# Kernel tuning notes

Measured on AMD Instinct MI355X. Metric: run time of the kernel, lower is better.

Reference implementation:

```python
import jax, jax.numpy as jnp
import numpy as np

C_CURV = 0.01   # manifold curvature c
EPS = 1e-7
KH = KW = 3
PAD = 1
STRIDE = 1


def log0(y):
    # Poincare-ball log map at origin: artanh(sqrt(c)||y||) * y / (sqrt(c)||y||)
    sqc = jnp.sqrt(jnp.asarray(C_CURV, y.dtype))
    n = jnp.maximum(jnp.linalg.norm(y, axis=-1, keepdims=True), EPS)
    return jnp.arctanh(jnp.clip(sqc * n, 0.0, 1.0 - 1e-6)) * y / (sqc * n)


def exp0(v):
    # Poincare-ball exp map at origin: tanh(sqrt(c)||v||) * v / (sqrt(c)||v||)
    sqc = jnp.sqrt(jnp.asarray(C_CURV, v.dtype))
    n = jnp.maximum(jnp.linalg.norm(v, axis=-1, keepdims=True), EPS)
    return jnp.tanh(sqc * n) * v / (sqc * n)


def setup_inputs() -> dict:
    key = jax.random.key(0)
    k1, k2, k3 = jax.random.split(key, 3)
    x = jax.random.uniform(k1, (4, 32, 256, 256), dtype=jnp.float32)  # points in ball (c=0.01 -> radius 10)
    Wk = jax.random.normal(k2, (KH * KW, 32, 32), dtype=jnp.float32) * 0.05  # [K, C_out, C_in]
    bias = jax.random.normal(k3, (32,), dtype=jnp.float32) * 0.01
    return {"x": x, "Wk": Wk, "bias": bias}


def reference(x, Wk, bias):
    B, Cin, H, W = x.shape
    Hout = (H + 2 * PAD - KH) // STRIDE + 1
    Wout = (W + 2 * PAD - KW) // STRIDE + 1
    xp = jnp.pad(x, ((0, 0), (0, 0), (PAD, PAD), (PAD, PAD)))
    # unfold: one slice per kernel position (i,j), matching F.unfold's (C_in, K, L) layout
    patches = jnp.stack(
        [xp[:, :, i:i + Hout * STRIDE:STRIDE, j:j + Wout * STRIDE:STRIDE]
         for i in range(KH) for j in range(KW)], axis=0)      # [K, B, Cin, Hout, Wout]
    u = log0(jnp.moveaxis(patches, 2, -1))                    # [K, B, Hout, Wout, Cin] tangent vectors
    # PVFC (mobius matvec = exp0(W @ log0(x))) followed by log0 cancels the exp0:
    # log0(PVFC_k(x)) = W_k @ log0(x). Aggregate (sum over k) fused into the einsum.
    v = jnp.einsum('kbhwc,koc->bhwo', u, Wk)                  # [B, Hout, Wout, Cout]
    v = jax.nn.relu(v + bias)
    out = exp0(v)                                             # back to manifold
    return jnp.transpose(out, (0, 3, 1, 2))                   # [B, Cout, Hout, Wout]
```

## Files before the change

### kernel.cpp

```cpp
#include <hip/hip_runtime.h>
#include <math.h>


#define TW 32
#define TH 8
#define HW_ 34
#define HH_ 10
#define NPIX 340
#define USTR 40
#define WSTR 40
#define VSTR 33
#define CIN 32
#define COUT 32

typedef __attribute__((ext_vector_type(8))) short bf16x8;
typedef __attribute__((ext_vector_type(4))) float f32x4;

__device__ inline unsigned short f2bf(float f) {
    unsigned int u = __builtin_bit_cast(unsigned int, f);
    unsigned int r = (u + 0x7FFFu + ((u >> 16) & 1u)) >> 16;
    return (unsigned short)r;
}

__global__ __launch_bounds__(256) void pvconv_kernel(
    const float* __restrict__ x, const float* __restrict__ Wk,
    const float* __restrict__ bias, float* __restrict__ out)
{
    __shared__ __align__(16) unsigned char smem[27200 + 23040];
    unsigned short* u  = (unsigned short*)smem;
    unsigned short* Wb = (unsigned short*)(smem + 27200);
    float*          v  = (float*)smem;

    const int t  = threadIdx.x;
    const int bx = blockIdx.x, by = blockIdx.y, b = blockIdx.z;
    const int x0 = bx * TW, y0 = by * TH;

    for (int e = t; e < 9 * 32 * 32; e += 256) {
        int tap = e >> 10, rem = e & 1023, o = rem >> 5, c = rem & 31;
        Wb[(tap * 32 + o) * WSTR + c] = f2bf(Wk[e]);
    }

    for (int p = t; p < NPIX; p += 256) {
        int py = p / HW_, px = p - py * HW_;
        int gy = y0 - 1 + py, gx = x0 - 1 + px;
        float vv[CIN];
        if ((unsigned)gy < 256u && (unsigned)gx < 256u) {
            const float* xp = x + (size_t)b * CIN * 65536 + gy * 256 + gx;
            #pragma unroll
            for (int c = 0; c < CIN; ++c) vv[c] = xp[(size_t)c * 65536];
        } else {
            #pragma unroll
            for (int c = 0; c < CIN; ++c) vv[c] = 0.f;
        }
        float ss = 0.f;
        #pragma unroll
        for (int c = 0; c < CIN; ++c) ss = fmaf(vv[c], vv[c], ss);
        float n = fmaxf(sqrtf(ss), 1e-7f);
        float z = fminf(0.1f * n, 1.f - 1e-6f);
        float at = 0.5f * logf((1.f + z) / (1.f - z));
        float s = at / (0.1f * n);
        unsigned int packed[16];
        #pragma unroll
        for (int c2 = 0; c2 < 16; ++c2)
            packed[c2] = (unsigned int)f2bf(vv[2 * c2] * s)
                       | ((unsigned int)f2bf(vv[2 * c2 + 1] * s) << 16);
        uint4* dst = (uint4*)&u[p * USTR];
        #pragma unroll
        for (int j = 0; j < 4; ++j) dst[j] = ((uint4*)packed)[j];
    }
    __syncthreads();

    const int wv = t >> 6, lane = t & 63;
    const int m = lane & 15, quad = lane >> 4;

    f32x4 acc[2][4];
    #pragma unroll
    for (int n = 0; n < 2; ++n)
        #pragma unroll
        for (int mt = 0; mt < 4; ++mt) acc[n][mt] = (f32x4)0.f;

    int abase[4];
    #pragma unroll
    for (int mt = 0; mt < 4; ++mt) {
        int pb = wv * 64 + mt * 16;
        int pxb = pb & 31, pyb = pb >> 5;
        abase[mt] = (pyb * HW_ + pxb + m) * USTR + quad * 8;
    }

    #pragma unroll
    for (int tap = 0; tap < 9; ++tap) {
        const int dy = tap / 3, dx = tap - dy * 3;
        const int hoff = (dy * HW_ + dx) * USTR;
        bf16x8 bf0 = *(const bf16x8*)&Wb[(tap * 32 + m) * WSTR + quad * 8];
        bf16x8 bf1 = *(const bf16x8*)&Wb[(tap * 32 + 16 + m) * WSTR + quad * 8];
        #pragma unroll
        for (int mt = 0; mt < 4; ++mt) {
            bf16x8 af = *(const bf16x8*)&u[abase[mt] + hoff];
            acc[0][mt] = __builtin_amdgcn_mfma_f32_16x16x32_bf16(af, bf0, acc[0][mt], 0, 0, 0);
            acc[1][mt] = __builtin_amdgcn_mfma_f32_16x16x32_bf16(af, bf1, acc[1][mt], 0, 0, 0);
        }
    }

    const float bia0 = bias[m], bia1 = bias[16 + m];
    __syncthreads();

    #pragma unroll
    for (int n = 0; n < 2; ++n)
        #pragma unroll
        for (int mt = 0; mt < 4; ++mt)
            #pragma unroll
            for (int r = 0; r < 4; ++r) {
                int pix = wv * 64 + mt * 16 + quad * 4 + r;
                int chan = n * 16 + m;
                float val = acc[n][mt][r] + (n ? bia1 : bia0);
                v[pix * VSTR + chan] = fmaxf(val, 0.f);
            }
    __syncthreads();

    {
        const int px = t & 31, py = t >> 5;
        float q[COUT];
        float ss = 0.f;
        #pragma unroll
        for (int o = 0; o < COUT; ++o) { q[o] = v[t * VSTR + o]; ss = fmaf(q[o], q[o], ss); }
        float n = fmaxf(sqrtf(ss), 1e-7f);
        float s = tanhf(0.1f * n) / (0.1f * n);
        const size_t base = (size_t)b * COUT * 65536 + (size_t)(y0 + py) * 256 + (x0 + px);
        #pragma unroll
        for (int o = 0; o < COUT; ++o)
            out[base + (size_t)o * 65536] = s * q[o];
    }
}

extern "C" void kernel_launch(void* const* d_in, const int* in_sizes, int n_in,
                              void* d_out, int out_size, void* d_ws, size_t ws_size,
                              hipStream_t stream) {
    const float* x    = (const float*)d_in[0];
    const float* Wk   = (const float*)d_in[1];
    const float* bias = (const float*)d_in[2];
    float* out = (float*)d_out;

    dim3 grid(256 / TW, 256 / TH, 4);
    dim3 block(256);
    pvconv_kernel<<<grid, block, 0, stream>>>(x, Wk, bias, out);
}
```

Baseline: 101.2 us.

## Swizzle LDS layout to shrink shared memory and raise occupancy

Replaces padded LDS strides with a compact 64-byte-row XOR-swizzled layout for the bf16 activations and weights. This cuts shared memory per block so more blocks can be resident (launch bounds now ask for 4 per CU) while avoiding bank conflicts. Weight conversion now uses vectorized float4 loads, the epilogue reads the staged output with float4 loads at a stride of 36, and logf/tanhf are replaced with fast intrinsics. The fast intrinsics may slightly change numerical accuracy, and the tighter register budget could cause spills.

```diff
diff --git a/kernel.cpp b/kernel.cpp
--- a/kernel.cpp
+++ b/kernel.cpp
@@ -5,13 +5,11 @@
 #define TW 32
 #define TH 8
 #define HW_ 34
-#define HH_ 10
 #define NPIX 340
-#define USTR 40
-#define WSTR 40
-#define VSTR 33
 #define CIN 32
 #define COUT 32
+#define U_BYTES 21760
+#define W_ROWS 288
 
 typedef __attribute__((ext_vector_type(8))) short bf16x8;
 typedef __attribute__((ext_vector_type(4))) float f32x4;
@@ -22,22 +20,30 @@
     return (unsigned short)r;
 }
 
-__global__ __launch_bounds__(256) void pvconv_kernel(
+__global__ __launch_bounds__(256, 4) void pvconv_kernel(
     const float* __restrict__ x, const float* __restrict__ Wk,
     const float* __restrict__ bias, float* __restrict__ out)
 {
-    __shared__ __align__(16) unsigned char smem[27200 + 23040];
-    unsigned short* u  = (unsigned short*)smem;
-    unsigned short* Wb = (unsigned short*)(smem + 27200);
-    float*          v  = (float*)smem;
+    __shared__ __align__(16) unsigned char smem[U_BYTES + W_ROWS * 64];
+    unsigned char* u8 = smem;
+    unsigned char* w8 = smem + U_BYTES;
+    float*         v  = (float*)smem;
 
     const int t  = threadIdx.x;
     const int bx = blockIdx.x, by = blockIdx.y, b = blockIdx.z;
     const int x0 = bx * TW, y0 = by * TH;
 
-    for (int e = t; e < 9 * 32 * 32; e += 256) {
-        int tap = e >> 10, rem = e & 1023, o = rem >> 5, c = rem & 31;
-        Wb[(tap * 32 + o) * WSTR + c] = f2bf(Wk[e]);
+    for (int f = t; f < W_ROWS * 4; f += 256) {
+        int r = f >> 2, j = f & 3;
+        const float4* src = (const float4*)(Wk + r * 32 + j * 8);
+        float4 a = src[0], c = src[1];
+        unsigned int pk[4];
+        pk[0] = (unsigned int)f2bf(a.x) | ((unsigned int)f2bf(a.y) << 16);
+        pk[1] = (unsigned int)f2bf(a.z) | ((unsigned int)f2bf(a.w) << 16);
+        pk[2] = (unsigned int)f2bf(c.x) | ((unsigned int)f2bf(c.y) << 16);
+        pk[3] = (unsigned int)f2bf(c.z) | ((unsigned int)f2bf(c.w) << 16);
+        int sw = j ^ ((r >> 1) & 3);
+        *(uint4*)(w8 + r * 64 + sw * 16) = *(uint4*)pk;
     }
 
     for (int p = t; p < NPIX; p += 256) {
@@ -57,16 +63,19 @@
         for (int c = 0; c < CIN; ++c) ss = fmaf(vv[c], vv[c], ss);
         float n = fmaxf(sqrtf(ss), 1e-7f);
         float z = fminf(0.1f * n, 1.f - 1e-6f);
-        float at = 0.5f * logf((1.f + z) / (1.f - z));
+        float at = 0.5f * __logf((1.f + z) / (1.f - z));
         float s = at / (0.1f * n);
-        unsigned int packed[16];
+        int swb = (p >> 1) & 3;
+        uint4* row = (uint4*)(u8 + p * 64);
         #pragma unroll
-        for (int c2 = 0; c2 < 16; ++c2)
-            packed[c2] = (unsigned int)f2bf(vv[2 * c2] * s)
-                       | ((unsigned int)f2bf(vv[2 * c2 + 1] * s) << 16);
-        uint4* dst = (uint4*)&u[p * USTR];
-        #pragma unroll
-        for (int j = 0; j < 4; ++j) dst[j] = ((uint4*)packed)[j];
+        for (int j = 0; j < 4; ++j) {
+            unsigned int pk[4];
+            #pragma unroll
+            for (int w = 0; w < 4; ++w)
+                pk[w] = (unsigned int)f2bf(vv[j * 8 + 2 * w] * s)
+                      | ((unsigned int)f2bf(vv[j * 8 + 2 * w + 1] * s) << 16);
+            row[j ^ swb] = *(uint4*)pk;
+        }
     }
     __syncthreads();
 
@@ -79,23 +88,25 @@
         #pragma unroll
         for (int mt = 0; mt < 4; ++mt) acc[n][mt] = (f32x4)0.f;
 
-    int abase[4];
+    int apix[4];
     #pragma unroll
     for (int mt = 0; mt < 4; ++mt) {
         int pb = wv * 64 + mt * 16;
-        int pxb = pb & 31, pyb = pb >> 5;
-        abase[mt] = (pyb * HW_ + pxb + m) * USTR + quad * 8;
+        apix[mt] = (pb >> 5) * HW_ + (pb & 31) + m;
     }
 
     #pragma unroll
     for (int tap = 0; tap < 9; ++tap) {
         const int dy = tap / 3, dx = tap - dy * 3;
-        const int hoff = (dy * HW_ + dx) * USTR;
-        bf16x8 bf0 = *(const bf16x8*)&Wb[(tap * 32 + m) * WSTR + quad * 8];
-        bf16x8 bf1 = *(const bf16x8*)&Wb[(tap * 32 + 16 + m) * WSTR + quad * 8];
+        const int hoff = dy * HW_ + dx;
+        int r0 = tap * 32 + m;
+        int swB = quad ^ ((r0 >> 1) & 3);
+        bf16x8 bf0 = *(const bf16x8*)(w8 + r0 * 64 + swB * 16);
+        bf16x8 bf1 = *(const bf16x8*)(w8 + (r0 + 16) * 64 + swB * 16);
         #pragma unroll
         for (int mt = 0; mt < 4; ++mt) {
-            bf16x8 af = *(const bf16x8*)&u[abase[mt] + hoff];
+            int hp = apix[mt] + hoff;
+            bf16x8 af = *(const bf16x8*)(u8 + hp * 64 + ((quad ^ ((hp >> 1) & 3)) << 4));
             acc[0][mt] = __builtin_amdgcn_mfma_f32_16x16x32_bf16(af, bf0, acc[0][mt], 0, 0, 0);
             acc[1][mt] = __builtin_amdgcn_mfma_f32_16x16x32_bf16(af, bf1, acc[1][mt], 0, 0, 0);
         }
@@ -111,20 +122,27 @@
             #pragma unroll
             for (int r = 0; r < 4; ++r) {
                 int pix = wv * 64 + mt * 16 + quad * 4 + r;
-                int chan = n * 16 + m;
                 float val = acc[n][mt][r] + (n ? bia1 : bia0);
-                v[pix * VSTR + chan] = fmaxf(val, 0.f);
+                v[pix * 36 + n * 16 + m] = fmaxf(val, 0.f);
             }
     __syncthreads();
 
     {
-        const int px = t & 31, py = t >> 5;
         float q[COUT];
+        const float4* vp = (const float4*)(smem + (size_t)t * 144);
+        #pragma unroll
+        for (int j = 0; j < 8; ++j) {
+            float4 c4 = vp[j];
+            q[4 * j] = c4.x; q[4 * j + 1] = c4.y; q[4 * j + 2] = c4.z; q[4 * j + 3] = c4.w;
+        }
         float ss = 0.f;
         #pragma unroll
-        for (int o = 0; o < COUT; ++o) { q[o] = v[t * VSTR + o]; ss = fmaf(q[o], q[o], ss); }
+        for (int o = 0; o < COUT; ++o) ss = fmaf(q[o], q[o], ss);
         float n = fmaxf(sqrtf(ss), 1e-7f);
-        float s = tanhf(0.1f * n) / (0.1f * n);
+        float a = 0.1f * n;
+        float e = __expf(-2.f * a);
+        float s = (1.f - e) / ((1.f + e) * a);
+        const int px = t & 31, py = t >> 5;
         const size_t base = (size_t)b * COUT * 65536 + (size_t)(y0 + py) * 256 + (x0 + px);
         #pragma unroll
         for (int o = 0; o < COUT; ++o)
```

After: 98.00 us. 1.03x faster.
